# Kernel optimization log

Hardware: AMD Instinct MI355X
Metric: run time of the kernel (lower is better)

The kernel has to match this reference:

```python
import jax, jax.numpy as jnp
import numpy as np

CHANNELS = 512
GROUPS = 32
EPS = 1e-5


def setup_inputs() -> dict:
    key = jax.random.key(0)
    ks = jax.random.split(key, 7)
    C = CHANNELS
    x = jax.random.normal(ks[0], (32, C, 32, 32), dtype=jnp.float32)
    norm_w = jax.random.normal(ks[1], (C,), dtype=jnp.float32) * 0.02 + 1.0
    norm_b = jax.random.normal(ks[2], (C,), dtype=jnp.float32) * 0.02
    # 1x1 convs stored as (out_channels, in_channels)
    qkv_w = jax.random.normal(ks[3], (3 * C, C), dtype=jnp.float32) * (C ** -0.5)
    qkv_b = jax.random.normal(ks[4], (3 * C,), dtype=jnp.float32) * 0.02
    proj_w = jax.random.normal(ks[5], (C, C), dtype=jnp.float32) * (C ** -0.5)
    proj_b = jax.random.normal(ks[6], (C,), dtype=jnp.float32) * 0.02
    return {"x": x, "norm_w": norm_w, "norm_b": norm_b,
            "qkv_w": qkv_w, "qkv_b": qkv_b,
            "proj_w": proj_w, "proj_b": proj_b}


def _group_norm(x, w, b):
    B, C, H, W = x.shape
    xg = x.reshape(B, GROUPS, C // GROUPS, H, W)
    mean = xg.mean(axis=(2, 3, 4), keepdims=True)
    var = xg.var(axis=(2, 3, 4), keepdims=True)
    xn = ((xg - mean) * jax.lax.rsqrt(var + EPS)).reshape(B, C, H, W)
    return xn * w[None, :, None, None] + b[None, :, None, None]


def reference(x, norm_w, norm_b, qkv_w, qkv_b, proj_w, proj_b):
    B, C, H, W = x.shape
    scale = C ** (-0.5)
    h = _group_norm(x, norm_w, norm_b)
    # 1x1 conv == per-pixel linear: (B,C,H,W) -> (B,3C,H,W)
    qkv = jnp.einsum('bchw,oc->bohw', h, qkv_w) + qkv_b[None, :, None, None]
    qkv = qkv.reshape(B, 3, C, H * W)
    q, k, v = qkv[:, 0], qkv[:, 1], qkv[:, 2]  # each (B, C, N)
    # attn[b, i, j] = softmax_j( q[:, i] . k[:, j] * scale )
    scores = jnp.einsum('bcn,bcm->bnm', q, k) * scale  # (B, N, N)
    attn = jax.nn.softmax(scores, axis=-1)
    # h[b, c, i] = sum_j v[b, c, j] * attn[b, i, j]
    hout = jnp.einsum('bcm,bnm->bcn', v, attn).reshape(B, C, H, W)
    out = x + jnp.einsum('bchw,oc->bohw', hout, proj_w) + proj_b[None, :, None, None]
    return out
```

## Files before the change

kernel.cpp:

```cpp
#include <hip/hip_runtime.h>
#include <math.h>

#define B_ 32
#define C_ 512
#define G_ 32
#define N_ 1024
#define OC3_ 1536
#define EPS_ 1e-5f

typedef __attribute__((ext_vector_type(8))) short short8;
typedef __attribute__((ext_vector_type(4))) float f32x4;

__device__ inline unsigned short f2bf(float f) {
    unsigned u = __builtin_bit_cast(unsigned, f);
    u += 0x7fffu + ((u >> 16) & 1u);
    return (unsigned short)(u >> 16);
}
__device__ inline unsigned pack2(float lo, float hi) {
    return (unsigned)f2bf(lo) | ((unsigned)f2bf(hi) << 16);
}
__device__ inline float bf2f(unsigned short u) {
    return __builtin_bit_cast(float, ((unsigned)u) << 16);
}

typedef const __attribute__((address_space(1))) unsigned int* gas_u32;
typedef __attribute__((address_space(3))) unsigned int* las_u32;
__device__ __forceinline__ void cp16(unsigned short* lds, const unsigned short* g) {
    __builtin_amdgcn_global_load_lds((gas_u32)g, (las_u32)lds, 16, 0, 0);
}

__global__ __launch_bounds__(256) void gn_stats_kernel(
    const float* __restrict__ x, float* __restrict__ stats)
{
    int bg = blockIdx.x;
    const float4* xv = (const float4*)(x + (size_t)bg * 16 * N_);
    float s = 0.f, ss = 0.f;
    for (int i = threadIdx.x; i < 4096; i += 256) {
        float4 v = xv[i];
        s  += v.x + v.y + v.z + v.w;
        ss += v.x*v.x + v.y*v.y + v.z*v.z + v.w*v.w;
    }
    __shared__ float r1[256], r2[256];
    r1[threadIdx.x] = s; r2[threadIdx.x] = ss;
    __syncthreads();
    for (int off = 128; off > 0; off >>= 1) {
        if (threadIdx.x < off) {
            r1[threadIdx.x] += r1[threadIdx.x + off];
            r2[threadIdx.x] += r2[threadIdx.x + off];
        }
        __syncthreads();
    }
    if (threadIdx.x == 0) {
        float mean = r1[0] * (1.f / 16384.f);
        float var  = r2[0] * (1.f / 16384.f) - mean * mean;
        stats[bg * 2 + 0] = mean;
        stats[bg * 2 + 1] = rsqrtf(var + EPS_);
    }
}

__global__ __launch_bounds__(256) void cvt_bf16_kernel(
    const float* __restrict__ src, unsigned short* __restrict__ dst, int n4)
{
    int i = blockIdx.x * 256 + threadIdx.x;
    if (i >= n4) return;
    float4 v = ((const float4*)src)[i];
    uint2 o; o.x = pack2(v.x, v.y); o.y = pack2(v.z, v.w);
    ((uint2*)dst)[i] = o;
}

__global__ __launch_bounds__(256) void hhatT_kernel(
    const float* __restrict__ x, const float* __restrict__ stats,
    const float* __restrict__ nw, const float* __restrict__ nbias,
    unsigned short* __restrict__ hhatT, long sH, int b0)
{
    int bz = blockIdx.z, b = b0 + bz;
    int nt = blockIdx.x * 64, ct = blockIdx.y * 64;
    const float* xb = x + (size_t)b * C_ * N_;
    const float* st = stats + b * 2 * G_;

    __shared__ float T[64][65];
    int tid = threadIdx.x;

    #pragma unroll
    for (int p = 0; p < 4; ++p) {
        int c = p * 16 + (tid >> 4);
        int n4 = (tid & 15) * 4;
        float4 v = *(const float4*)&xb[(size_t)(ct + c) * N_ + nt + n4];
        int g = (ct + c) >> 4;
        float w0 = nw[ct + c] * st[g * 2 + 1];
        float bb = nbias[ct + c] - st[g * 2] * w0;
        T[c][n4]   = v.x * w0 + bb;
        T[c][n4+1] = v.y * w0 + bb;
        T[c][n4+2] = v.z * w0 + bb;
        T[c][n4+3] = v.w * w0 + bb;
    }
    __syncthreads();
    #pragma unroll
    for (int p = 0; p < 2; ++p) {
        int n  = p * 32 + (tid >> 3);
        int c8 = (tid & 7) * 8;
        short8 s;
        #pragma unroll
        for (int u = 0; u < 8; ++u) s[u] = (short)f2bf(T[c8 + u][n]);
        *(short8*)&hhatT[(size_t)bz * sH + (size_t)(nt + n) * C_ + ct + c8] = s;
    }
}

template<int EPI>
__global__ __launch_bounds__(256) void gemm128(
    const unsigned short* __restrict__ A, long sA, int lda,
    const unsigned short* __restrict__ B, long sB, int ldb,
    void* __restrict__ Dv, long sD, int ldd,
    const float* __restrict__ bias,
    const float* __restrict__ aux, long sAux,
    int K, float scale, int gx, int gy, int nbz)
{
    int bid = blockIdx.x;
    int nbpb = gx * gy;
    int bx, by, bz;
    if ((nbz & 7) == 0) {
        int xcd = bid & 7;
        int rest = bid >> 3;
        int local = rest % nbpb;
        int bg = rest / nbpb;
        bz = bg * 8 + xcd;
        bx = local % gx;
        by = local / gx;
    } else {
        bz = bid / nbpb;
        int local = bid % nbpb;
        bx = local % gx;
        by = local / gx;
    }

    const unsigned short* Ab = A + (size_t)bz * sA + (size_t)bx * 128 * lda;
    const unsigned short* Bb = B + (size_t)bz * sB + (size_t)by * 128 * ldb;

    __shared__ __align__(16) unsigned short As[2][128 * 32];
    __shared__ __align__(16) unsigned short Bs[2][128 * 32];

    int tid = threadIdx.x;
    int w = tid >> 6, lane = tid & 63;
    int lm = lane & 15, q = lane >> 4;
    int wrow = (w >> 1) * 64, wcol = (w & 1) * 64;

    f32x4 acc[4][4];
    #pragma unroll
    for (int i = 0; i < 4; ++i)
        #pragma unroll
        for (int j = 0; j < 4; ++j) acc[i][j] = (f32x4)(0.f);

    int srow = tid >> 2;
    int skc  = (((tid & 3) ^ ((tid >> 3) & 3))) * 8;
    int fco  = (q ^ ((lm >> 1) & 3)) * 8;

    const unsigned short* a0p = Ab + (size_t)srow        * lda + skc;
    const unsigned short* a1p = Ab + (size_t)(64 + srow) * lda + skc;
    const unsigned short* b0p = Bb + (size_t)srow        * ldb + skc;
    const unsigned short* b1p = Bb + (size_t)(64 + srow) * ldb + skc;

    cp16(&As[0][tid * 8],        a0p);
    cp16(&As[0][2048 + tid * 8], a1p);
    cp16(&Bs[0][tid * 8],        b0p);
    cp16(&Bs[0][2048 + tid * 8], b1p);

    int nIter = K >> 5;
    for (int it = 0; it < nIter; ++it) {
        int cur = it & 1;
        __syncthreads();
        if (it + 1 < nIter) {
            int off = (it + 1) * 32;
            int nxt = cur ^ 1;
            cp16(&As[nxt][tid * 8],        a0p + off);
            cp16(&As[nxt][2048 + tid * 8], a1p + off);
            cp16(&Bs[nxt][tid * 8],        b0p + off);
            cp16(&Bs[nxt][2048 + tid * 8], b1p + off);
        }
        short8 af[4], bf[4];
        #pragma unroll
        for (int i = 0; i < 4; ++i)
            af[i] = *(const short8*)&As[cur][(wrow + i * 16 + lm) * 32 + fco];
        #pragma unroll
        for (int j = 0; j < 4; ++j)
            bf[j] = *(const short8*)&Bs[cur][(wcol + j * 16 + lm) * 32 + fco];
        #pragma unroll
        for (int i = 0; i < 4; ++i)
            #pragma unroll
            for (int j = 0; j < 4; ++j)
                acc[i][j] = __builtin_amdgcn_mfma_f32_16x16x32_bf16(
                    af[i], bf[j], acc[i][j], 0, 0, 0);
    }

    int grow = bx * 128 + wrow;
    int gcol = by * 128 + wcol;

    #pragma unroll
    for (int j = 0; j < 4; ++j) {
        int col = gcol + j * 16 + lm;
        float cb = (EPI == 0) ? bias[col] : 0.f;
        #pragma unroll
        for (int i = 0; i < 4; ++i) {
            #pragma unroll
            for (int r = 0; r < 4; ++r) {
                int row = grow + i * 16 + q * 4 + r;
                float vle = acc[i][j][r];
                if constexpr (EPI == 0) {
                    vle += cb;
                    ((unsigned short*)Dv)[(size_t)bz * sD + (size_t)row * ldd + col] = f2bf(vle);
                } else if constexpr (EPI == 1) {
                    vle += bias[row];
                    ((unsigned short*)Dv)[(size_t)bz * sD + (size_t)row * ldd + col] = f2bf(vle);
                } else if constexpr (EPI == 2) {
                    ((unsigned short*)Dv)[(size_t)bz * sD + (size_t)row * ldd + col] = f2bf(vle * scale);
                } else if constexpr (EPI == 3) {
                    ((unsigned short*)Dv)[(size_t)bz * sD + (size_t)row * ldd + col] = f2bf(vle);
                } else {
                    vle += bias[row] + aux[(size_t)bz * sAux + (size_t)row * ldd + col];
                    ((float*)Dv)[(size_t)bz * sD + (size_t)row * ldd + col] = vle;
                }
            }
        }
    }
}

__global__ __launch_bounds__(256) void softmax_kernel(
    unsigned short* __restrict__ sc, long sSc)
{
    int bz = blockIdx.y;
    int row = blockIdx.x * 4 + (threadIdx.x >> 6);
    int lane = threadIdx.x & 63;
    unsigned short* p = sc + (size_t)bz * sSc + (size_t)row * N_ + lane * 16;

    short8 s0 = *(const short8*)p;
    short8 s1 = *(const short8*)(p + 8);
    float v[16];
    #pragma unroll
    for (int i = 0; i < 8; ++i) {
        v[i]     = bf2f((unsigned short)s0[i]);
        v[8 + i] = bf2f((unsigned short)s1[i]);
    }
    float m = v[0];
    #pragma unroll
    for (int i = 1; i < 16; ++i) m = fmaxf(m, v[i]);
    #pragma unroll
    for (int off = 32; off > 0; off >>= 1) m = fmaxf(m, __shfl_xor(m, off, 64));

    float sum = 0.f;
    #pragma unroll
    for (int i = 0; i < 16; ++i) { v[i] = __expf(v[i] - m); sum += v[i]; }
    #pragma unroll
    for (int off = 32; off > 0; off >>= 1) sum += __shfl_xor(sum, off, 64);
    float inv = 1.f / sum;

    short8 o0, o1;
    #pragma unroll
    for (int i = 0; i < 8; ++i) {
        o0[i] = (short)f2bf(v[i] * inv);
        o1[i] = (short)f2bf(v[8 + i] * inv);
    }
    *(short8*)p = o0;
    *(short8*)(p + 8) = o1;
}

extern "C" void kernel_launch(void* const* d_in, const int* in_sizes, int n_in,
                              void* d_out, int out_size, void* d_ws, size_t ws_size,
                              hipStream_t stream) {
    const float* x      = (const float*)d_in[0];
    const float* norm_w = (const float*)d_in[1];
    const float* norm_b = (const float*)d_in[2];
    const float* qkv_w  = (const float*)d_in[3];
    const float* qkv_b  = (const float*)d_in[4];
    const float* proj_w = (const float*)d_in[5];
    const float* proj_b = (const float*)d_in[6];
    float* out = (float*)d_out;

    char* ws = (char*)d_ws;
    float* stats = (float*)ws;
    unsigned short* wqkv  = (unsigned short*)(ws + 8192);
    unsigned short* wproj = wqkv + (size_t)OC3_ * C_;
    char* base = (char*)(wproj + (size_t)C_ * C_);
    const size_t fixed = 8192 + (size_t)OC3_ * C_ * 2 + (size_t)C_ * C_ * 2;

    const size_t REG = 6u << 20;
    const long RSH = (long)(REG / 2);

    size_t avail = ws_size > fixed ? ws_size - fixed : 0;
    int chunk = (int)(avail / REG);
    if (chunk < 1) chunk = 1;
    if (chunk > B_) chunk = B_;

    gn_stats_kernel<<<dim3(B_ * G_), dim3(256), 0, stream>>>(x, stats);
    cvt_bf16_kernel<<<dim3((OC3_ * C_ / 4 + 255) / 256), dim3(256), 0, stream>>>(
        qkv_w, wqkv, OC3_ * C_ / 4);
    cvt_bf16_kernel<<<dim3((C_ * C_ / 4 + 255) / 256), dim3(256), 0, stream>>>(
        proj_w, wproj, C_ * C_ / 4);

    const float scale = 0.044194173824159216f;

    unsigned short* qkT   = (unsigned short*)base;
    unsigned short* vbuf  = (unsigned short*)(base + (2u << 20));
    unsigned short* hhatT = (unsigned short*)(base + (3u << 20));
    unsigned short* houtT = (unsigned short*)(base + (3u << 20));
    unsigned short* sc    = (unsigned short*)(base + (4u << 20));

    for (int b0 = 0; b0 < B_; b0 += chunk) {
        int nb = B_ - b0 < chunk ? B_ - b0 : chunk;

        hhatT_kernel<<<dim3(N_/64, C_/64, nb), dim3(256), 0, stream>>>(
            x, stats, norm_w, norm_b, hhatT, RSH, b0);

        gemm128<0><<<dim3(8 * 8 * nb), dim3(256), 0, stream>>>(
            hhatT, RSH, C_,  wqkv, 0, C_,
            qkT, RSH, 1024,  qkv_b, nullptr, 0, C_, 0.f, 8, 8, nb);

        gemm128<1><<<dim3(4 * 8 * nb), dim3(256), 0, stream>>>(
            wqkv + (size_t)1024 * C_, 0, C_,  hhatT, RSH, C_,
            vbuf, RSH, N_,  qkv_b + 1024, nullptr, 0, C_, 0.f, 4, 8, nb);

        gemm128<2><<<dim3(8 * 8 * nb), dim3(256), 0, stream>>>(
            qkT, RSH, 1024,  qkT + 512, RSH, 1024,
            sc, RSH, N_,  nullptr, nullptr, 0, C_, scale, 8, 8, nb);

        softmax_kernel<<<dim3(N_/4, nb), dim3(256), 0, stream>>>(sc, RSH);

        gemm128<3><<<dim3(8 * 4 * nb), dim3(256), 0, stream>>>(
            sc, RSH, N_,  vbuf, RSH, N_,
            houtT, RSH, C_,  nullptr, nullptr, 0, N_, 0.f, 8, 4, nb);

        gemm128<4><<<dim3(4 * 8 * nb), dim3(256), 0, stream>>>(
            wproj, 0, C_,  houtT, RSH, C_,
            out + (size_t)b0 * C_ * N_, (long)C_ * N_, N_,
            proj_b, x + (size_t)b0 * C_ * N_, (long)C_ * N_, C_, 0.f, 4, 8, nb);
    }
}
```

Before: 408.5 us.

## Replace 128x128 GEMM with 256x256-tile, 8-wave, 4-stage pipelined GEMM

Grows the shared GEMM kernel's block tile from 128x128 to 256x256, using 512 threads (8 waves, each computing 128x64) and a 4-buffer LDS ring that prefetches two K-steps ahead. Explicit vmcnt/lgkmcnt waits, split barriers, sched_barrier and setprio interleave the async copies with the MFMA work. The goal is more data reuse per LDS load and better hiding of global-load latency. The cost is 4x fewer blocks per launch, which may leave CUs idle at small batch chunks, plus higher register pressure from 32 accumulators per thread.

```diff
diff --git a/kernel.cpp b/kernel.cpp
--- a/kernel.cpp
+++ b/kernel.cpp
@@ -107,7 +107,7 @@
 }
 
 template<int EPI>
-__global__ __launch_bounds__(256) void gemm128(
+__global__ __launch_bounds__(512) void gemm256(
     const unsigned short* __restrict__ A, long sA, int lda,
     const unsigned short* __restrict__ B, long sB, int ldb,
     void* __restrict__ Dv, long sD, int ldd,
@@ -133,77 +133,105 @@
         by = local / gx;
     }
 
-    const unsigned short* Ab = A + (size_t)bz * sA + (size_t)bx * 128 * lda;
-    const unsigned short* Bb = B + (size_t)bz * sB + (size_t)by * 128 * ldb;
-
-    __shared__ __align__(16) unsigned short As[2][128 * 32];
-    __shared__ __align__(16) unsigned short Bs[2][128 * 32];
+    const unsigned short* Ab = A + (size_t)bz * sA + (size_t)bx * 256 * lda;
+    const unsigned short* Bb = B + (size_t)bz * sB + (size_t)by * 256 * ldb;
+
+    __shared__ __align__(16) unsigned short lds[4][2][8192];
 
     int tid = threadIdx.x;
-    int w = tid >> 6, lane = tid & 63;
-    int lm = lane & 15, q = lane >> 4;
-    int wrow = (w >> 1) * 64, wcol = (w & 1) * 64;
-
-    f32x4 acc[4][4];
-    #pragma unroll
-    for (int i = 0; i < 4; ++i)
+    int w = tid >> 6, l = tid & 63;
+    int wm = w >> 2, wn = w & 3;
+    int wrow = wm * 128, wcol = wn * 64;
+    int lm = l & 15, q = l >> 4;
+
+    f32x4 acc[8][4];
+    #pragma unroll
+    for (int i = 0; i < 8; ++i)
         #pragma unroll
         for (int j = 0; j < 4; ++j) acc[i][j] = (f32x4)(0.f);
 
-    int srow = tid >> 2;
-    int skc  = (((tid & 3) ^ ((tid >> 3) & 3))) * 8;
-    int fco  = (q ^ ((lm >> 1) & 3)) * 8;
-
-    const unsigned short* a0p = Ab + (size_t)srow        * lda + skc;
-    const unsigned short* a1p = Ab + (size_t)(64 + srow) * lda + skc;
-    const unsigned short* b0p = Bb + (size_t)srow        * ldb + skc;
-    const unsigned short* b1p = Bb + (size_t)(64 + srow) * ldb + skc;
-
-    cp16(&As[0][tid * 8],        a0p);
-    cp16(&As[0][2048 + tid * 8], a1p);
-    cp16(&Bs[0][tid * 8],        b0p);
-    cp16(&Bs[0][2048 + tid * 8], b1p);
-
-    int nIter = K >> 5;
-    for (int it = 0; it < nIter; ++it) {
-        int cur = it & 1;
-        __syncthreads();
-        if (it + 1 < nIter) {
-            int off = (it + 1) * 32;
-            int nxt = cur ^ 1;
-            cp16(&As[nxt][tid * 8],        a0p + off);
-            cp16(&As[nxt][2048 + tid * 8], a1p + off);
-            cp16(&Bs[nxt][tid * 8],        b0p + off);
-            cp16(&Bs[nxt][2048 + tid * 8], b1p + off);
+    int srow = l >> 2;
+    int gch  = (l & 3) ^ ((l >> 3) & 3);
+    const unsigned short* aS0 = Ab + (size_t)(w * 32 +      srow) * lda + gch * 8;
+    const unsigned short* aS1 = Ab + (size_t)(w * 32 + 16 + srow) * lda + gch * 8;
+    const unsigned short* bS0 = Bb + (size_t)(w * 32 +      srow) * ldb + gch * 8;
+    const unsigned short* bS1 = Bb + (size_t)(w * 32 + 16 + srow) * ldb + gch * 8;
+    int ld0 = w * 1024 + l * 8;
+    int ld1 = w * 1024 + 512 + l * 8;
+
+    int fch = (q ^ ((lm >> 1) & 3)) * 8;
+    int aro = (wrow + lm) * 32 + fch;
+    int bro = (wcol + lm) * 32 + fch;
+
+    cp16(&lds[0][0][ld0], aS0);      cp16(&lds[0][0][ld1], aS1);
+    cp16(&lds[0][1][ld0], bS0);      cp16(&lds[0][1][ld1], bS1);
+    cp16(&lds[1][0][ld0], aS0 + 32); cp16(&lds[1][0][ld1], aS1 + 32);
+    cp16(&lds[1][1][ld0], bS0 + 32); cp16(&lds[1][1][ld1], bS1 + 32);
+    asm volatile("s_waitcnt vmcnt(4)" ::: "memory");
+    __builtin_amdgcn_s_barrier();
+
+    int nt = K >> 5;
+    for (int t = 0; t < nt; ++t) {
+        const unsigned short* At = &lds[t & 3][0][0];
+        const unsigned short* Bt = &lds[t & 3][1][0];
+        bool stg = (t + 2) < nt;
+        int sb = (t + 2) & 3;
+        int so = (t + 2) * 32;
+
+        short8 bf[4];
+        #pragma unroll
+        for (int ph = 0; ph < 2; ++ph) {
+            short8 af[4];
+            #pragma unroll
+            for (int m = 0; m < 4; ++m)
+                af[m] = *(const short8*)&At[aro + (ph * 64 + m * 16) * 32];
+            if (ph == 0) {
+                #pragma unroll
+                for (int n = 0; n < 4; ++n)
+                    bf[n] = *(const short8*)&Bt[bro + n * 16 * 32];
+                if (stg) {
+                    cp16(&lds[sb][0][ld0], aS0 + so);
+                    cp16(&lds[sb][0][ld1], aS1 + so);
+                }
+            } else {
+                if (stg) {
+                    cp16(&lds[sb][1][ld0], bS0 + so);
+                    cp16(&lds[sb][1][ld1], bS1 + so);
+                }
+            }
+            __builtin_amdgcn_s_barrier();
+            asm volatile("s_waitcnt lgkmcnt(0)" ::: "memory");
+            __builtin_amdgcn_sched_barrier(0);
+            __builtin_amdgcn_s_setprio(1);
+            #pragma unroll
+            for (int m = 0; m < 4; ++m)
+                #pragma unroll
+                for (int n = 0; n < 4; ++n)
+                    acc[ph * 4 + m][n] = __builtin_amdgcn_mfma_f32_16x16x32_bf16(
+                        af[m], bf[n], acc[ph * 4 + m][n], 0, 0, 0);
+            __builtin_amdgcn_s_setprio(0);
+            __builtin_amdgcn_sched_barrier(0);
+            if (ph == 1 && t + 1 < nt) {
+                if (t + 2 < nt) asm volatile("s_waitcnt vmcnt(4)" ::: "memory");
+                else            asm volatile("s_waitcnt vmcnt(0)" ::: "memory");
+            }
+            __builtin_amdgcn_s_barrier();
         }
-        short8 af[4], bf[4];
-        #pragma unroll
-        for (int i = 0; i < 4; ++i)
-            af[i] = *(const short8*)&As[cur][(wrow + i * 16 + lm) * 32 + fco];
-        #pragma unroll
-        for (int j = 0; j < 4; ++j)
-            bf[j] = *(const short8*)&Bs[cur][(wcol + j * 16 + lm) * 32 + fco];
-        #pragma unroll
-        for (int i = 0; i < 4; ++i)
-            #pragma unroll
-            for (int j = 0; j < 4; ++j)
-                acc[i][j] = __builtin_amdgcn_mfma_f32_16x16x32_bf16(
-                    af[i], bf[j], acc[i][j], 0, 0, 0);
-    }
-
-    int grow = bx * 128 + wrow;
-    int gcol = by * 128 + wcol;
-
-    #pragma unroll
-    for (int j = 0; j < 4; ++j) {
-        int col = gcol + j * 16 + lm;
+    }
+
+    int grow = bx * 256 + wrow;
+    int gcol = by * 256 + wcol;
+
+    #pragma unroll
+    for (int n = 0; n < 4; ++n) {
+        int col = gcol + n * 16 + lm;
         float cb = (EPI == 0) ? bias[col] : 0.f;
         #pragma unroll
-        for (int i = 0; i < 4; ++i) {
+        for (int mi = 0; mi < 8; ++mi) {
             #pragma unroll
             for (int r = 0; r < 4; ++r) {
-                int row = grow + i * 16 + q * 4 + r;
-                float vle = acc[i][j][r];
+                int row = grow + mi * 16 + q * 4 + r;
+                float vle = acc[mi][n][r];
                 if constexpr (EPI == 0) {
                     vle += cb;
                     ((unsigned short*)Dv)[(size_t)bz * sD + (size_t)row * ldd + col] = f2bf(vle);
@@ -309,27 +337,27 @@
         hhatT_kernel<<<dim3(N_/64, C_/64, nb), dim3(256), 0, stream>>>(
             x, stats, norm_w, norm_b, hhatT, RSH, b0);
 
-        gemm128<0><<<dim3(8 * 8 * nb), dim3(256), 0, stream>>>(
+        gemm256<0><<<dim3(4 * 4 * nb), dim3(512), 0, stream>>>(
             hhatT, RSH, C_,  wqkv, 0, C_,
-            qkT, RSH, 1024,  qkv_b, nullptr, 0, C_, 0.f, 8, 8, nb);
-
-        gemm128<1><<<dim3(4 * 8 * nb), dim3(256), 0, stream>>>(
+            qkT, RSH, 1024,  qkv_b, nullptr, 0, C_, 0.f, 4, 4, nb);
+
+        gemm256<1><<<dim3(2 * 4 * nb), dim3(512), 0, stream>>>(
             wqkv + (size_t)1024 * C_, 0, C_,  hhatT, RSH, C_,
-            vbuf, RSH, N_,  qkv_b + 1024, nullptr, 0, C_, 0.f, 4, 8, nb);
-
-        gemm128<2><<<dim3(8 * 8 * nb), dim3(256), 0, stream>>>(
+            vbuf, RSH, N_,  qkv_b + 1024, nullptr, 0, C_, 0.f, 2, 4, nb);
+
+        gemm256<2><<<dim3(4 * 4 * nb), dim3(512), 0, stream>>>(
             qkT, RSH, 1024,  qkT + 512, RSH, 1024,
-            sc, RSH, N_,  nullptr, nullptr, 0, C_, scale, 8, 8, nb);
+            sc, RSH, N_,  nullptr, nullptr, 0, C_, scale, 4, 4, nb);
 
         softmax_kernel<<<dim3(N_/4, nb), dim3(256), 0, stream>>>(sc, RSH);
 
-        gemm128<3><<<dim3(8 * 4 * nb), dim3(256), 0, stream>>>(
+        gemm256<3><<<dim3(4 * 2 * nb), dim3(512), 0, stream>>>(
             sc, RSH, N_,  vbuf, RSH, N_,
-            houtT, RSH, C_,  nullptr, nullptr, 0, N_, 0.f, 8, 4, nb);
-
-        gemm128<4><<<dim3(4 * 8 * nb), dim3(256), 0, stream>>>(
+            houtT, RSH, C_,  nullptr, nullptr, 0, N_, 0.f, 4, 2, nb);
+
+        gemm256<4><<<dim3(2 * 4 * nb), dim3(512), 0, stream>>>(
             wproj, 0, C_,  houtT, RSH, C_,
             out + (size_t)b0 * C_ * N_, (long)C_ * N_, N_,
-            proj_b, x + (size_t)b0 * C_ * N_, (long)C_ * N_, C_, 0.f, 4, 8, nb);
-    }
-}
+            proj_b, x + (size_t)b0 * C_ * N_, (long)C_ * N_, C_, 0.f, 2, 4, nb);
+    }
+}
```

Result: slower. 462.8 us (+13.3%).
